# Kernel optimization log

Measured on AMD Instinct MI355X. Metric: run time of the kernel, lower is better.

## Reference

```python
import jax, jax.numpy as jnp
import numpy as np

BN_EPS = 1e-5


def setup_inputs() -> dict:
    key = jax.random.key(0)
    ks = jax.random.split(key, 12)
    N, E = 100000, 500000
    NF, IF, OF = 128, 32, 128  # node_features, in_features, out_features
    x = jax.random.normal(ks[0], (N, NF), dtype=jnp.float32)
    edge_index = jax.random.randint(ks[1], (2, E), 0, N, dtype=jnp.int64)
    edge_attr = jax.random.normal(ks[2], (E, IF), dtype=jnp.float32)
    # input_layer: Linear(IF, OF)
    W1 = jax.random.normal(ks[3], (IF, OF), dtype=jnp.float32) / np.sqrt(IF)
    b1 = jnp.zeros((OF,), dtype=jnp.float32)
    # mlp Linear(OF + 2*NF, NF)
    W2 = jax.random.normal(ks[4], (OF + 2 * NF, NF), dtype=jnp.float32) / np.sqrt(OF + 2 * NF)
    b2 = jnp.zeros((NF,), dtype=jnp.float32)
    # BatchNorm(NF) params + running stats (eval mode)
    bn_gamma = jnp.ones((NF,), dtype=jnp.float32)
    bn_beta = jnp.zeros((NF,), dtype=jnp.float32)
    bn_mean = 0.1 * jax.random.normal(ks[5], (NF,), dtype=jnp.float32)
    bn_var = 0.5 + jax.random.uniform(ks[6], (NF,), dtype=jnp.float32)
    # mlp Linear(NF, OF)
    W3 = jax.random.normal(ks[7], (NF, OF), dtype=jnp.float32) / np.sqrt(NF)
    b3 = jnp.zeros((OF,), dtype=jnp.float32)
    return {
        "x": x, "edge_index": edge_index, "edge_attr": edge_attr,
        "W1": W1, "b1": b1, "W2": W2, "b2": b2,
        "bn_gamma": bn_gamma, "bn_beta": bn_beta,
        "bn_mean": bn_mean, "bn_var": bn_var,
        "W3": W3, "b3": b3,
    }


def reference(x, edge_index, edge_attr, W1, b1, W2, b2, bn_gamma, bn_beta, bn_mean, bn_var, W3, b3):
    # input_layer: Linear + Tanh  -> [E, OF]
    e = jnp.tanh(edge_attr @ W1 + b1)
    row, col = edge_index[0], edge_index[1]
    # gather + concat -> [E, 2*NF + OF]
    h = jnp.concatenate([x[row], x[col], e], axis=1)
    # Linear -> BatchNorm (eval, running stats) -> ReLU -> Dropout(eval=id)
    h = h @ W2 + b2
    h = (h - bn_mean) * (bn_gamma / jnp.sqrt(bn_var + BN_EPS)) + bn_beta
    h = jax.nn.relu(h)
    # Linear -> ReLU -> [E, OF]
    y = jax.nn.relu(h @ W3 + b3)
    return y
```

## Files before the change

### kernel.cpp

```cpp
#include <hip/hip_runtime.h>

typedef __attribute__((ext_vector_type(4))) float f32x4;
typedef __attribute__((ext_vector_type(8))) short s16x8;

static __device__ __forceinline__ unsigned short f2bf(float f){
  unsigned int u = __builtin_bit_cast(unsigned int, f);
  u = (u + 0x7fffu + ((u >> 16) & 1u)) >> 16;
  return (unsigned short)u;
}
static __device__ __forceinline__ float bf2f(unsigned short s){
  unsigned int u = ((unsigned int)s) << 16;
  return __builtin_bit_cast(float, u);
}
static __device__ __forceinline__ float tanh_fast(float x){
  float ex = __expf(2.0f * x);
  return 1.0f - 2.0f * __builtin_amdgcn_rcpf(ex + 1.0f);
}

__global__ void prep_kernel(const float* __restrict__ W1, const float* __restrict__ W2,
                            const float* __restrict__ W3, const float* __restrict__ b2,
                            const float* __restrict__ g, const float* __restrict__ be,
                            const float* __restrict__ mn, const float* __restrict__ vr,
                            unsigned short* __restrict__ w1p, unsigned short* __restrict__ w2cp,
                            unsigned short* __restrict__ w3p, float* __restrict__ bnsc,
                            float* __restrict__ bnsh)
{
  int t = blockIdx.x * blockDim.x + threadIdx.x;
  int nt = gridDim.x * blockDim.x;
  for (int idx = t; idx < 4096; idx += nt){
    int i = idx & 7, lane = (idx >> 3) & 63, n0 = idx >> 9;
    w1p[idx] = f2bf(W1[((lane >> 4) * 8 + i) * 128 + n0 * 16 + (lane & 15)]);
  }
  for (int idx = t; idx < 16384; idx += nt){
    int i = idx & 7, lane = (idx >> 3) & 63, n0 = (idx >> 9) & 7, kk = idx >> 12;
    int k = kk * 32 + (lane >> 4) * 8 + i;
    int j = n0 * 16 + (lane & 15);
    w2cp[idx] = f2bf(W2[(size_t)(256 + k) * 128 + j]);
    w3p[idx]  = f2bf(W3[(size_t)k * 128 + j]);
  }
  for (int idx = t; idx < 128; idx += nt){
    float sc = g[idx] * rsqrtf(vr[idx] + 1e-5f);
    bnsc[idx] = sc;
    bnsh[idx] = (b2[idx] - mn[idx]) * sc + be[idx];
  }
}

__global__ __launch_bounds__(256) void node_kernel(
    const float* __restrict__ x, const float* __restrict__ W2,
    unsigned short* __restrict__ P, unsigned short* __restrict__ Q, int N)
{
  __shared__ __align__(16) float xs[32 * 132];
  __shared__ __align__(16) float wsm[32 * 256];
  const int tid = threadIdx.x;
  const int nb = blockIdx.x * 32;
  #pragma unroll
  for (int i = 0; i < 4; i++){
    int idx = i * 1024 + tid * 4;
    int row = idx >> 7, col = idx & 127;
    int n = nb + row; if (n >= N) n = N - 1;
    *(f32x4*)&xs[row * 132 + col] = *(const f32x4*)&x[(size_t)n * 128 + col];
  }
  float acc[32];
  #pragma unroll
  for (int a = 0; a < 32; a++) acc[a] = 0.f;
  const int jg = tid & 7, nl = tid >> 3;
  for (int kc = 0; kc < 4; kc++){
    __syncthreads();
    #pragma unroll
    for (int i = 0; i < 8; i++){
      int idx = i * 1024 + tid * 4;
      int k = idx >> 8, j = idx & 255;
      const float* src = (j < 128) ? &W2[(size_t)(kc * 32 + k) * 128 + j]
                                   : &W2[(size_t)(128 + kc * 32 + k) * 128 + (j - 128)];
      *(f32x4*)&wsm[k * 256 + j] = *(const f32x4*)src;
    }
    __syncthreads();
    #pragma unroll 8
    for (int k = 0; k < 32; k++){
      float xv = xs[nl * 132 + kc * 32 + k];
      #pragma unroll
      for (int q = 0; q < 4; q++){
        f32x4 wp = *(const f32x4*)&wsm[k * 256 + jg * 4 + q * 32];
        f32x4 wq = *(const f32x4*)&wsm[k * 256 + 128 + jg * 4 + q * 32];
        #pragma unroll
        for (int ii = 0; ii < 4; ii++){
          acc[q * 4 + ii]      = fmaf(xv, wp[ii], acc[q * 4 + ii]);
          acc[16 + q * 4 + ii] = fmaf(xv, wq[ii], acc[16 + q * 4 + ii]);
        }
      }
    }
  }
  const int n = nb + nl;
  if (n < N){
    #pragma unroll
    for (int q = 0; q < 4; q++){
      uint2 v;
      v.x = (unsigned int)f2bf(acc[q*4+0]) | ((unsigned int)f2bf(acc[q*4+1]) << 16);
      v.y = (unsigned int)f2bf(acc[q*4+2]) | ((unsigned int)f2bf(acc[q*4+3]) << 16);
      *(uint2*)&P[(size_t)n * 128 + jg * 4 + q * 32] = v;
      v.x = (unsigned int)f2bf(acc[16+q*4+0]) | ((unsigned int)f2bf(acc[16+q*4+1]) << 16);
      v.y = (unsigned int)f2bf(acc[16+q*4+2]) | ((unsigned int)f2bf(acc[16+q*4+3]) << 16);
      *(uint2*)&Q[(size_t)n * 128 + jg * 4 + q * 32] = v;
    }
  }
}

__global__ __launch_bounds__(256) void edge_kernel(
    const float* __restrict__ ea, const int* __restrict__ eidx,
    const unsigned short* __restrict__ P, const unsigned short* __restrict__ Q,
    const unsigned short* __restrict__ w1p, const unsigned short* __restrict__ w2cp,
    const unsigned short* __restrict__ w3p,
    const float* __restrict__ b1, const float* __restrict__ b3,
    const float* __restrict__ bnsc, const float* __restrict__ bnsh,
    float* __restrict__ y, int E, int N)
{
  __shared__ __align__(16) unsigned short w1f[4096];
  __shared__ __align__(16) unsigned short w2cf[16384];
  __shared__ __align__(16) unsigned short tch[4][32 * 40];
  __shared__ float cb1[128], cb3[128], cbs[128], cbh[128];

  const int tid = threadIdx.x;
  {
    const uint4* s1 = (const uint4*)w1p; uint4* d1 = (uint4*)w1f;
    d1[tid] = s1[tid];
    d1[tid + 256] = s1[tid + 256];
    const uint4* s2 = (const uint4*)w2cp; uint4* d2 = (uint4*)w2cf;
    #pragma unroll
    for (int i = 0; i < 8; i++) d2[tid + i * 256] = s2[tid + i * 256];
    if (tid < 128){ cb1[tid] = b1[tid]; cb3[tid] = b3[tid]; cbs[tid] = bnsc[tid]; cbh[tid] = bnsh[tid]; }
  }
  __syncthreads();

  const int wid = tid >> 6, lane = tid & 63;
  const int r16 = lane & 15, hi = lane >> 4;
  const int e0 = (blockIdx.x * 4 + wid) * 32;
  unsigned short* myt = &tch[wid][0];

  s16x8 aF[2];
  #pragma unroll
  for (int m = 0; m < 2; m++){
    int e = e0 + m * 16 + r16; if (e >= E) e = E - 1;
    const f32x4* p = (const f32x4*)(ea + (size_t)e * 32 + hi * 8);
    f32x4 v0 = p[0], v1 = p[1];
    s16x8 t;
    t[0] = (short)f2bf(v0[0]); t[1] = (short)f2bf(v0[1]); t[2] = (short)f2bf(v0[2]); t[3] = (short)f2bf(v0[3]);
    t[4] = (short)f2bf(v1[0]); t[5] = (short)f2bf(v1[1]); t[6] = (short)f2bf(v1[2]); t[7] = (short)f2bf(v1[3]);
    aF[m] = t;
  }

  const s16x8* w1fv = (const s16x8*)w1f;
  const s16x8* w2cfv = (const s16x8*)w2cf;
  const f32x4 z = {0.f, 0.f, 0.f, 0.f};

  f32x4 c2[2][8];
  #pragma unroll
  for (int m = 0; m < 2; m++)
    #pragma unroll
    for (int n0 = 0; n0 < 8; n0++) c2[m][n0] = z;

  #pragma unroll
  for (int kk = 0; kk < 4; kk++){
    f32x4 t1[2][2];
    #pragma unroll
    for (int j2 = 0; j2 < 2; j2++){
      s16x8 bF = w1fv[(kk * 2 + j2) * 64 + lane];
      t1[0][j2] = __builtin_amdgcn_mfma_f32_16x16x32_bf16(aF[0], bF, z, 0, 0, 0);
      t1[1][j2] = __builtin_amdgcn_mfma_f32_16x16x32_bf16(aF[1], bF, z, 0, 0, 0);
    }
    #pragma unroll
    for (int j2 = 0; j2 < 2; j2++){
      const int n0t = kk * 2 + j2;
      const float bb = cb1[n0t * 16 + r16];
      #pragma unroll
      for (int m = 0; m < 2; m++){
        #pragma unroll
        for (int r = 0; r < 4; r++){
          float tv = tanh_fast(t1[m][j2][r] + bb);
          myt[(m * 16 + hi * 4 + r) * 40 + j2 * 16 + r16] = f2bf(tv);
        }
      }
    }
    s16x8 a2[2];
    #pragma unroll
    for (int m = 0; m < 2; m++)
      a2[m] = *(const s16x8*)(myt + (m * 16 + r16) * 40 + hi * 8);
    #pragma unroll
    for (int n0 = 0; n0 < 8; n0++){
      s16x8 bF = w2cfv[(kk * 8 + n0) * 64 + lane];
      c2[0][n0] = __builtin_amdgcn_mfma_f32_16x16x32_bf16(a2[0], bF, c2[0][n0], 0, 0, 0);
      c2[1][n0] = __builtin_amdgcn_mfma_f32_16x16x32_bf16(a2[1], bF, c2[1][n0], 0, 0, 0);
    }
  }

  int rowi[2][4], coli[2][4];
  #pragma unroll
  for (int m = 0; m < 2; m++){
    #pragma unroll
    for (int r = 0; r < 4; r++){
      int em = e0 + m * 16 + hi * 4 + r; if (em >= E) em = E - 1;
      int ri = eidx[em];     ri = (ri < 0) ? 0 : (ri >= N ? N - 1 : ri);
      int ci = eidx[E + em]; ci = (ci < 0) ? 0 : (ci >= N ? N - 1 : ci);
      rowi[m][r] = ri; coli[m][r] = ci;
    }
  }

  f32x4 c3[2][8];
  #pragma unroll
  for (int m = 0; m < 2; m++)
    #pragma unroll
    for (int n0 = 0; n0 < 8; n0++) c3[m][n0] = z;

  const uint4* w3g = (const uint4*)w3p;
  #pragma unroll
  for (int kk = 0; kk < 4; kk++){
    #pragma unroll
    for (int j2 = 0; j2 < 2; j2++){
      const int n0 = kk * 2 + j2;
      const float sc = cbs[n0 * 16 + r16], sh = cbh[n0 * 16 + r16];
      #pragma unroll
      for (int m = 0; m < 2; m++){
        #pragma unroll
        for (int r = 0; r < 4; r++){
          float hv = c2[m][n0][r]
            + bf2f(P[(size_t)rowi[m][r] * 128 + n0 * 16 + r16])
            + bf2f(Q[(size_t)coli[m][r] * 128 + n0 * 16 + r16]);
          hv = fmaf(hv, sc, sh);
          hv = fmaxf(hv, 0.0f);
          myt[(m * 16 + hi * 4 + r) * 40 + j2 * 16 + r16] = f2bf(hv);
        }
      }
    }
    s16x8 a3[2];
    #pragma unroll
    for (int m = 0; m < 2; m++)
      a3[m] = *(const s16x8*)(myt + (m * 16 + r16) * 40 + hi * 8);
    #pragma unroll
    for (int n0 = 0; n0 < 8; n0++){
      uint4 bu = w3g[(kk * 8 + n0) * 64 + lane];
      union { uint4 u; s16x8 s; } cv; cv.u = bu;
      c3[0][n0] = __builtin_amdgcn_mfma_f32_16x16x32_bf16(a3[0], cv.s, c3[0][n0], 0, 0, 0);
      c3[1][n0] = __builtin_amdgcn_mfma_f32_16x16x32_bf16(a3[1], cv.s, c3[1][n0], 0, 0, 0);
    }
  }

  #pragma unroll
  for (int m = 0; m < 2; m++){
    #pragma unroll
    for (int r = 0; r < 4; r++){
      int em = e0 + m * 16 + hi * 4 + r;
      if (em < E){
        float* yp = y + (size_t)em * 128 + r16;
        #pragma unroll
        for (int n0 = 0; n0 < 8; n0++)
          yp[n0 * 16] = fmaxf(c3[m][n0][r] + cb3[n0 * 16 + r16], 0.0f);
      }
    }
  }
}

extern "C" void kernel_launch(void* const* d_in, const int* in_sizes, int n_in,
                              void* d_out, int out_size, void* d_ws, size_t ws_size,
                              hipStream_t stream)
{
  const float* x    = (const float*)d_in[0];
  const int*   eidx = (const int*)d_in[1];
  const float* ea   = (const float*)d_in[2];
  const float* W1   = (const float*)d_in[3];
  const float* b1   = (const float*)d_in[4];
  const float* W2   = (const float*)d_in[5];
  const float* b2   = (const float*)d_in[6];
  const float* bng  = (const float*)d_in[7];
  const float* bnb  = (const float*)d_in[8];
  const float* bnm  = (const float*)d_in[9];
  const float* bnv  = (const float*)d_in[10];
  const float* W3   = (const float*)d_in[11];
  const float* b3   = (const float*)d_in[12];
  float* y = (float*)d_out;
  const int N = in_sizes[0] / 128;
  const int E = in_sizes[2] / 32;

  unsigned short* P    = (unsigned short*)d_ws;
  unsigned short* Qq   = P + (size_t)N * 128;
  unsigned short* w1p  = Qq + (size_t)N * 128;
  unsigned short* w2cp = w1p + 4096;
  unsigned short* w3p  = w2cp + 16384;
  float* bnsc = (float*)(w3p + 16384);
  float* bnsh = bnsc + 128;

  hipLaunchKernelGGL(prep_kernel, dim3(64), dim3(256), 0, stream,
                     W1, W2, W3, b2, bng, bnb, bnm, bnv, w1p, w2cp, w3p, bnsc, bnsh);
  hipLaunchKernelGGL(node_kernel, dim3((N + 31) / 32), dim3(256), 0, stream, x, W2, P, Qq, N);
  hipLaunchKernelGGL(edge_kernel, dim3((E + 127) / 128), dim3(256), 0, stream,
                     ea, eidx, P, Qq, w1p, w2cp, w3p, b1, b3, bnsc, bnsh, y, E, N);
}
```

Before: 630.1 us.

## Prefetch P/Q rows as vector loads in A-fragment layout before weight staging

The kernel now loads each edge's P and Q rows up front with 16-byte vector loads that already match the MFMA A-fragment layout, issued before the shared-memory weight staging so their latency overlaps it. Previously every element was gathered with scalar 2-byte loads in the accumulator layout. To combine these with the layer-2 accumulator, the full 32x128 intermediate is written to a larger per-wave LDS tile and read back transposed, and a launch-bounds occupancy hint of 2 is added. The trade-off is more register pressure from the held prefetch data, more LDS per block, and an extra bf16 rounding of the accumulator before the bias/BN step.

```diff
diff --git a/kernel.cpp b/kernel.cpp
--- a/kernel.cpp
+++ b/kernel.cpp
@@ -105,7 +105,7 @@
   }
 }
 
-__global__ __launch_bounds__(256) void edge_kernel(
+__global__ __launch_bounds__(256, 2) void edge_kernel(
     const float* __restrict__ ea, const int* __restrict__ eidx,
     const unsigned short* __restrict__ P, const unsigned short* __restrict__ Q,
     const unsigned short* __restrict__ w1p, const unsigned short* __restrict__ w2cp,
@@ -116,25 +116,34 @@
 {
   __shared__ __align__(16) unsigned short w1f[4096];
   __shared__ __align__(16) unsigned short w2cf[16384];
-  __shared__ __align__(16) unsigned short tch[4][32 * 40];
+  __shared__ __align__(16) unsigned short tch[4][32 * 136];
   __shared__ float cb1[128], cb3[128], cbs[128], cbh[128];
 
   const int tid = threadIdx.x;
-  {
-    const uint4* s1 = (const uint4*)w1p; uint4* d1 = (uint4*)w1f;
-    d1[tid] = s1[tid];
-    d1[tid + 256] = s1[tid + 256];
-    const uint4* s2 = (const uint4*)w2cp; uint4* d2 = (uint4*)w2cf;
-    #pragma unroll
-    for (int i = 0; i < 8; i++) d2[tid + i * 256] = s2[tid + i * 256];
-    if (tid < 128){ cb1[tid] = b1[tid]; cb3[tid] = b3[tid]; cbs[tid] = bnsc[tid]; cbh[tid] = bnsh[tid]; }
-  }
-  __syncthreads();
-
   const int wid = tid >> 6, lane = tid & 63;
   const int r16 = lane & 15, hi = lane >> 4;
   const int e0 = (blockIdx.x * 4 + wid) * 32;
   unsigned short* myt = &tch[wid][0];
+
+  int ri[2], ci[2];
+  #pragma unroll
+  for (int m = 0; m < 2; m++){
+    int e = e0 + m * 16 + r16; if (e >= E) e = E - 1;
+    int r = eidx[e];     r = (r < 0) ? 0 : (r >= N ? N - 1 : r);
+    int c = eidx[E + e]; c = (c < 0) ? 0 : (c >= N ? N - 1 : c);
+    ri[m] = r; ci[m] = c;
+  }
+  uint4 pg[2][4], qg[2][4];
+  #pragma unroll
+  for (int m = 0; m < 2; m++){
+    const uint4* pr = (const uint4*)(P + (size_t)ri[m] * 128 + hi * 8);
+    const uint4* qr = (const uint4*)(Q + (size_t)ci[m] * 128 + hi * 8);
+    #pragma unroll
+    for (int kk = 0; kk < 4; kk++){
+      pg[m][kk] = pr[kk * 4];
+      qg[m][kk] = qr[kk * 4];
+    }
+  }
 
   s16x8 aF[2];
   #pragma unroll
@@ -148,6 +157,17 @@
     aF[m] = t;
   }
 
+  {
+    const uint4* s1 = (const uint4*)w1p; uint4* d1 = (uint4*)w1f;
+    d1[tid] = s1[tid];
+    d1[tid + 256] = s1[tid + 256];
+    const uint4* s2 = (const uint4*)w2cp; uint4* d2 = (uint4*)w2cf;
+    #pragma unroll
+    for (int i = 0; i < 8; i++) d2[tid + i * 256] = s2[tid + i * 256];
+    if (tid < 128){ cb1[tid] = b1[tid]; cb3[tid] = b3[tid]; cbs[tid] = bnsc[tid]; cbh[tid] = bnsh[tid]; }
+  }
+  __syncthreads();
+
   const s16x8* w1fv = (const s16x8*)w1f;
   const s16x8* w2cfv = (const s16x8*)w2cf;
   const f32x4 z = {0.f, 0.f, 0.f, 0.f};
@@ -176,14 +196,14 @@
         #pragma unroll
         for (int r = 0; r < 4; r++){
           float tv = tanh_fast(t1[m][j2][r] + bb);
-          myt[(m * 16 + hi * 4 + r) * 40 + j2 * 16 + r16] = f2bf(tv);
+          myt[(m * 16 + hi * 4 + r) * 136 + j2 * 16 + r16] = f2bf(tv);
         }
       }
     }
     s16x8 a2[2];
     #pragma unroll
     for (int m = 0; m < 2; m++)
-      a2[m] = *(const s16x8*)(myt + (m * 16 + r16) * 40 + hi * 8);
+      a2[m] = *(const s16x8*)(myt + (m * 16 + r16) * 136 + hi * 8);
     #pragma unroll
     for (int n0 = 0; n0 < 8; n0++){
       s16x8 bF = w2cfv[(kk * 8 + n0) * 64 + lane];
@@ -192,17 +212,13 @@
     }
   }
 
-  int rowi[2][4], coli[2][4];
-  #pragma unroll
-  for (int m = 0; m < 2; m++){
-    #pragma unroll
-    for (int r = 0; r < 4; r++){
-      int em = e0 + m * 16 + hi * 4 + r; if (em >= E) em = E - 1;
-      int ri = eidx[em];     ri = (ri < 0) ? 0 : (ri >= N ? N - 1 : ri);
-      int ci = eidx[E + em]; ci = (ci < 0) ? 0 : (ci >= N ? N - 1 : ci);
-      rowi[m][r] = ri; coli[m][r] = ci;
-    }
-  }
+  #pragma unroll
+  for (int m = 0; m < 2; m++)
+    #pragma unroll
+    for (int n0 = 0; n0 < 8; n0++)
+      #pragma unroll
+      for (int r = 0; r < 4; r++)
+        myt[(m * 16 + hi * 4 + r) * 136 + n0 * 16 + r16] = f2bf(c2[m][n0][r]);
 
   f32x4 c3[2][8];
   #pragma unroll
@@ -213,27 +229,28 @@
   const uint4* w3g = (const uint4*)w3p;
   #pragma unroll
   for (int kk = 0; kk < 4; kk++){
-    #pragma unroll
-    for (int j2 = 0; j2 < 2; j2++){
-      const int n0 = kk * 2 + j2;
-      const float sc = cbs[n0 * 16 + r16], sh = cbh[n0 * 16 + r16];
+    f32x4 sc0 = *(const f32x4*)&cbs[kk * 32 + hi * 8];
+    f32x4 sc1 = *(const f32x4*)&cbs[kk * 32 + hi * 8 + 4];
+    f32x4 sh0 = *(const f32x4*)&cbh[kk * 32 + hi * 8];
+    f32x4 sh1 = *(const f32x4*)&cbh[kk * 32 + hi * 8 + 4];
+    s16x8 a3[2];
+    #pragma unroll
+    for (int m = 0; m < 2; m++){
+      s16x8 ch = *(const s16x8*)(myt + (m * 16 + r16) * 136 + kk * 32 + hi * 8);
+      union { uint4 u; unsigned short s[8]; } pu, qu;
+      pu.u = pg[m][kk]; qu.u = qg[m][kk];
+      s16x8 t;
       #pragma unroll
-      for (int m = 0; m < 2; m++){
-        #pragma unroll
-        for (int r = 0; r < 4; r++){
-          float hv = c2[m][n0][r]
-            + bf2f(P[(size_t)rowi[m][r] * 128 + n0 * 16 + r16])
-            + bf2f(Q[(size_t)coli[m][r] * 128 + n0 * 16 + r16]);
-          hv = fmaf(hv, sc, sh);
-          hv = fmaxf(hv, 0.0f);
-          myt[(m * 16 + hi * 4 + r) * 40 + j2 * 16 + r16] = f2bf(hv);
-        }
+      for (int i = 0; i < 8; i++){
+        float hv = bf2f((unsigned short)ch[i]) + bf2f(pu.s[i]) + bf2f(qu.s[i]);
+        float sc = (i < 4) ? sc0[i] : sc1[i - 4];
+        float sh = (i < 4) ? sh0[i] : sh1[i - 4];
+        hv = fmaf(hv, sc, sh);
+        hv = fmaxf(hv, 0.0f);
+        t[i] = (short)f2bf(hv);
       }
-    }
-    s16x8 a3[2];
-    #pragma unroll
-    for (int m = 0; m < 2; m++)
-      a3[m] = *(const s16x8*)(myt + (m * 16 + r16) * 40 + hi * 8);
+      a3[m] = t;
+    }
     #pragma unroll
     for (int n0 = 0; n0 < 8; n0++){
       uint4 bu = w3g[(kk * 8 + n0) * 64 + lane];
```

Result: faster. 566.5 us (-10.1%).
